# Kernel tuning notes

Hardware: AMD Instinct MI355X
Metric: run time of the kernel (lower is better)

Reference implementation:

```python
import jax, jax.numpy as jnp
import numpy as np

N, M, K = 262144, 65536, 32
C_IN, C_OUT = 64, 128
BN_EPS = 1e-5


def setup_inputs() -> dict:
    key = jax.random.key(0)
    ks = jax.random.split(key, 6)
    p = jax.random.normal(ks[0], (N, 3), jnp.float32)
    x = jax.random.normal(ks[1], (N, C_IN), jnp.float32)
    o = jnp.array([N], jnp.int32)  # single-cloud batch offsets
    idx = jnp.sort(jax.random.randint(ks[2], (M,), 0, N))  # sampled point indices (FPS stand-in)
    knn_idx = jax.random.randint(ks[3], (M, K), 0, N)      # neighbor indices (ball-query/knn stand-in)
    # learned params: Linear(C_IN+3 -> C_OUT) + BatchNorm1d(C_OUT)
    W = jax.random.normal(ks[4], (C_IN + 3, C_OUT), jnp.float32) / np.sqrt(C_IN + 3).astype(np.float32)
    b = jnp.zeros((C_OUT,), jnp.float32)
    gamma = jnp.ones((C_OUT,), jnp.float32)
    beta = jnp.zeros((C_OUT,), jnp.float32)
    return dict(p=p, x=x, o=o, idx=idx, knn_idx=knn_idx, W=W, b=b, gamma=gamma, beta=beta)


def reference(p, x, o, idx, knn_idx, W, b, gamma, beta):
    # sampler: n_p = p[idx]
    n_p = p[idx]  # [M, 3]
    # pooling with with_xyz=True: gather K neighbors, concat relative xyz, max-pool over K
    rel = p[knn_idx] - n_p[:, None, :]                      # [M, K, 3]
    grouped = jnp.concatenate([rel, x[knn_idx]], axis=-1)   # [M, K, 3+C_IN]
    pooled = grouped.max(axis=1)                            # [M, 3+C_IN]
    # convs: Linear -> BatchNorm1d (training-mode batch stats) -> ReLU
    h = pooled @ W + b                                      # [M, C_OUT]
    mean = h.mean(axis=0)
    var = h.var(axis=0)
    h = (h - mean) * jax.lax.rsqrt(var + BN_EPS) * gamma + beta
    x_out = jnp.maximum(h, 0.0)
    n_o = jnp.array([idx.shape[0]], jnp.int32)
    return (n_p, x_out, n_o)
```

## Files before the change

### kernel.cpp

```cpp
#include <hip/hip_runtime.h>
#include <hip/hip_fp16.h>
#include <math.h>

#define K_NB  32
#define C_IN  64
#define C_OUT 128
#define KP    96
#define TILE  128

typedef _Float16 f16x8 __attribute__((ext_vector_type(8)));
typedef float    f32x4 __attribute__((ext_vector_type(4)));

__device__ __forceinline__ float2 u2f2(unsigned u) {
    __half2 h = *reinterpret_cast<__half2*>(&u);
    return __half22float2(h);
}
__device__ __forceinline__ unsigned pk(float a, float b) {
    __half2 h = __floats2half2_rn(a, b);
    return *reinterpret_cast<unsigned*>(&h);
}

__global__ __launch_bounds__(256) void sa_zero(float* __restrict__ g, int n)
{
    for (int i = threadIdx.x; i < n; i += 256) g[i] = 0.f;
}

__global__ __launch_bounds__(256) void sa_cvt(
    const float4* __restrict__ x4, uint2* __restrict__ xh, int n4)
{
    for (int i = blockIdx.x * blockDim.x + threadIdx.x; i < n4;
         i += gridDim.x * blockDim.x) {
        float4 v = x4[i];
        xh[i] = make_uint2(pk(v.x, v.y), pk(v.z, v.w));
    }
}

__global__ __launch_bounds__(256) void sa_pool_h(
    const float* __restrict__ p, const uint4* __restrict__ xh4,
    const int* __restrict__ idx, const int* __restrict__ knn,
    float* __restrict__ np_out, float* __restrict__ hbuf)
{
    const int lane = threadIdx.x & 63;
    const int m    = blockIdx.x * 4 + (threadIdx.x >> 6);

    int kidx = 0;
    if (lane < K_NB) kidx = knn[m * K_NB + lane];

    float mx[8];
    #pragma unroll
    for (int j = 0; j < 8; ++j) mx[j] = -INFINITY;

    const int sub = lane & 7;
    #pragma unroll
    for (int i = 0; i < 4; ++i) {
        int nb = __shfl(kidx, i * 8 + (lane >> 3));
        uint4 u = xh4[(size_t)nb * 8 + sub];
        float2 f0 = u2f2(u.x), f1 = u2f2(u.y), f2 = u2f2(u.z), f3 = u2f2(u.w);
        mx[0] = fmaxf(mx[0], f0.x); mx[1] = fmaxf(mx[1], f0.y);
        mx[2] = fmaxf(mx[2], f1.x); mx[3] = fmaxf(mx[3], f1.y);
        mx[4] = fmaxf(mx[4], f2.x); mx[5] = fmaxf(mx[5], f2.y);
        mx[6] = fmaxf(mx[6], f3.x); mx[7] = fmaxf(mx[7], f3.y);
    }
    #pragma unroll
    for (int off = 8; off <= 32; off <<= 1)
        #pragma unroll
        for (int j = 0; j < 8; ++j)
            mx[j] = fmaxf(mx[j], __shfl_xor(mx[j], off));

    float px = -INFINITY, py = -INFINITY, pz = -INFINITY;
    if (lane < K_NB) {
        const float* pp = p + (size_t)kidx * 3;
        px = pp[0]; py = pp[1]; pz = pp[2];
    }
    #pragma unroll
    for (int off = 32; off >= 1; off >>= 1) {
        px = fmaxf(px, __shfl_xor(px, off));
        py = fmaxf(py, __shfl_xor(py, off));
        pz = fmaxf(pz, __shfl_xor(pz, off));
    }

    const int s = idx[m];
    const float npx = p[(size_t)s*3+0];
    const float npy = p[(size_t)s*3+1];
    const float npz = p[(size_t)s*3+2];
    if (lane < 3) np_out[(size_t)m*3 + lane] = (lane == 0) ? npx : (lane == 1 ? npy : npz);

    const int tile = m >> 7, rl = m & (TILE - 1);
    __half* rowh = (__half*)(hbuf + (size_t)tile * TILE * C_OUT) + rl * KP;
    if (lane < 8) {
        *(uint4*)(rowh + lane * 8) =
            make_uint4(pk(mx[0],mx[1]), pk(mx[2],mx[3]), pk(mx[4],mx[5]), pk(mx[6],mx[7]));
    } else if (lane == 8) {
        *(uint4*)(rowh + 64) = make_uint4(pk(px-npx, py-npy), pk(pz-npz, 0.f), 0u, 0u);
    } else if (lane < 12) {
        *(uint4*)(rowh + 64 + (lane - 8) * 8) = make_uint4(0u, 0u, 0u, 0u);
    }
}

__global__ __launch_bounds__(256) void sa_pool_f(
    const float* __restrict__ p, const float* __restrict__ x,
    const int* __restrict__ idx, const int* __restrict__ knn,
    float* __restrict__ np_out, float* __restrict__ hbuf)
{
    const int lane = threadIdx.x & 63;
    const int m    = blockIdx.x * 4 + (threadIdx.x >> 6);
    int kidx = 0;
    if (lane < K_NB) kidx = knn[m * K_NB + lane];
    float xmax = -INFINITY;
    #pragma unroll
    for (int k = 0; k < K_NB; ++k) {
        int nb = __shfl(kidx, k);
        xmax = fmaxf(xmax, x[(size_t)nb * C_IN + lane]);
    }
    float px = -INFINITY, py = -INFINITY, pz = -INFINITY;
    if (lane < K_NB) {
        const float* pp = p + (size_t)kidx * 3;
        px = pp[0]; py = pp[1]; pz = pp[2];
    }
    #pragma unroll
    for (int off = 32; off >= 1; off >>= 1) {
        px = fmaxf(px, __shfl_xor(px, off));
        py = fmaxf(py, __shfl_xor(py, off));
        pz = fmaxf(pz, __shfl_xor(pz, off));
    }
    const int s = idx[m];
    const float npx = p[(size_t)s*3], npy = p[(size_t)s*3+1], npz = p[(size_t)s*3+2];
    if (lane < 3) np_out[(size_t)m*3 + lane] = (lane == 0) ? npx : (lane == 1 ? npy : npz);

    const int tile = m >> 7, rl = m & (TILE - 1);
    __half* rowh = (__half*)(hbuf + (size_t)tile * TILE * C_OUT) + rl * KP;
    if (lane < 8) {
        float v[8];
        #pragma unroll
        for (int j = 0; j < 8; ++j) v[j] = __shfl(xmax, lane * 8 + j);
        *(uint4*)(rowh + lane * 8) =
            make_uint4(pk(v[0],v[1]), pk(v[2],v[3]), pk(v[4],v[5]), pk(v[6],v[7]));
    } else if (lane == 8) {
        *(uint4*)(rowh + 64) = make_uint4(pk(px-npx, py-npy), pk(pz-npz, 0.f), 0u, 0u);
    } else if (lane < 12) {
        *(uint4*)(rowh + 64 + (lane - 8) * 8) = make_uint4(0u, 0u, 0u, 0u);
    }
}

__global__ __launch_bounds__(256) void sa_gemm_mfma(
    const float* __restrict__ W, const float* __restrict__ bias,
    float* __restrict__ h, float* __restrict__ gsum, unsigned rep_mask)
{
    __shared__ __half Wt[C_OUT][128];
    __shared__ float reds[16][C_OUT];
    __shared__ float redq[16][C_OUT];

    const int t    = threadIdx.x;
    const int wave = t >> 6, lane = t & 63;
    const int l15  = lane & 15, lg = lane >> 4;
    const int m0   = blockIdx.x * TILE;

    for (int e = t; e < C_OUT * KP; e += 256) {
        const int c = e & 127, kk = e >> 7;
        float w = 0.f;
        if (kk < C_IN)          w = W[(size_t)(3 + kk) * C_OUT + c];
        else if (kk < C_IN + 3) w = W[(size_t)(kk - C_IN) * C_OUT + c];
        Wt[c][(((kk >> 3) ^ (c & 7)) << 3) | (kk & 7)] = __float2half(w);
    }

    const __half* tb = (const __half*)(h + (size_t)blockIdx.x * TILE * C_OUT);
    f16x8 A[2][3];
    #pragma unroll
    for (int rt = 0; rt < 2; ++rt) {
        const int rl = wave * 32 + rt * 16 + l15;
        #pragma unroll
        for (int ks = 0; ks < 3; ++ks)
            A[rt][ks] = *(const f16x8*)(tb + (size_t)rl * KP + ks * 32 + lg * 8);
    }
    __syncthreads();

    f32x4 acc[2][8];
    #pragma unroll
    for (int ct = 0; ct < 8; ++ct) {
        const float bc = bias[ct * 16 + l15];
        acc[0][ct] = (f32x4){bc, bc, bc, bc};
        acc[1][ct] = (f32x4){bc, bc, bc, bc};
    }
    #pragma unroll
    for (int ks = 0; ks < 3; ++ks) {
        #pragma unroll
        for (int ct = 0; ct < 8; ++ct) {
            const int c  = ct * 16 + l15;
            const int kc = ks * 4 + lg;
            const f16x8 wf = *(const f16x8*)&Wt[c][((kc ^ (c & 7)) << 3)];
            acc[0][ct] = __builtin_amdgcn_mfma_f32_16x16x32_f16(A[0][ks], wf, acc[0][ct], 0, 0, 0);
            acc[1][ct] = __builtin_amdgcn_mfma_f32_16x16x32_f16(A[1][ks], wf, acc[1][ct], 0, 0, 0);
        }
    }

    float s8[8], q8[8];
    #pragma unroll
    for (int ct = 0; ct < 8; ++ct) { s8[ct] = 0.f; q8[ct] = 0.f; }
    #pragma unroll
    for (int rt = 0; rt < 2; ++rt) {
        #pragma unroll
        for (int ct = 0; ct < 8; ++ct) {
            const int col = ct * 16 + l15;
            #pragma unroll
            for (int r = 0; r < 4; ++r) {
                const int row = m0 + wave * 32 + rt * 16 + lg * 4 + r;
                const float v = acc[rt][ct][r];
                h[(size_t)row * C_OUT + col] = v;
                s8[ct] += v;
                q8[ct]  = fmaf(v, v, q8[ct]);
            }
        }
    }
    #pragma unroll
    for (int ct = 0; ct < 8; ++ct) {
        reds[wave * 4 + lg][ct * 16 + l15] = s8[ct];
        redq[wave * 4 + lg][ct * 16 + l15] = q8[ct];
    }
    __syncthreads();
    if (t < C_OUT) {
        float ss = 0.f, qq = 0.f;
        #pragma unroll
        for (int i = 0; i < 16; ++i) { ss += reds[i][t]; qq += redq[i][t]; }
        float* g = gsum + (size_t)(blockIdx.x & rep_mask) * 2 * C_OUT;
        atomicAdd(&g[t],         ss);
        atomicAdd(&g[C_OUT + t], qq);
    }
}

__global__ __launch_bounds__(128) void sa_finalize(
    const float* __restrict__ gsum, const float* __restrict__ gamma,
    const float* __restrict__ beta, float* __restrict__ ss,
    float* __restrict__ no_out, int M, int rep)
{
    const int j = threadIdx.x;
    float s = 0.f, s2 = 0.f;
    for (int r = 0; r < rep; ++r) {
        s  += gsum[(size_t)r * 2 * C_OUT + j];
        s2 += gsum[(size_t)r * 2 * C_OUT + C_OUT + j];
    }
    const float inv_m = 1.0f / (float)M;
    const float mean = s * inv_m;
    const float var  = fmaf(-mean, mean, s2 * inv_m);
    const float sc   = gamma[j] * rsqrtf(var + 1e-5f);
    ss[j]         = sc;
    ss[C_OUT + j] = fmaf(-mean, sc, beta[j]);
    if (j == 0) no_out[0] = (float)M;
}

__global__ __launch_bounds__(256) void sa_bnrelu(
    float* __restrict__ h, const float* __restrict__ ss, int M)
{
    __shared__ float sc[C_OUT], sh[C_OUT];
    if (threadIdx.x < C_OUT) {
        sc[threadIdx.x] = ss[threadIdx.x];
        sh[threadIdx.x] = ss[C_OUT + threadIdx.x];
    }
    __syncthreads();
    const size_t total4 = (size_t)M * C_OUT / 4;
    float4* h4 = (float4*)h;
    for (size_t i = (size_t)blockIdx.x * blockDim.x + threadIdx.x;
         i < total4; i += (size_t)gridDim.x * blockDim.x) {
        float4 v = h4[i];
        const int c = (int)((i * 4) & (C_OUT - 1));
        v.x = fmaxf(fmaf(v.x, sc[c+0], sh[c+0]), 0.f);
        v.y = fmaxf(fmaf(v.y, sc[c+1], sh[c+1]), 0.f);
        v.z = fmaxf(fmaf(v.z, sc[c+2], sh[c+2]), 0.f);
        v.w = fmaxf(fmaf(v.w, sc[c+3], sh[c+3]), 0.f);
        h4[i] = v;
    }
}

extern "C" void kernel_launch(void* const* d_in, const int* in_sizes, int n_in,
                              void* d_out, int out_size, void* d_ws, size_t ws_size,
                              hipStream_t stream)
{
    const float* p     = (const float*)d_in[0];
    const float* x     = (const float*)d_in[1];
    const int*   idx   = (const int*)d_in[3];
    const int*   knn   = (const int*)d_in[4];
    const float* W     = (const float*)d_in[5];
    const float* bias  = (const float*)d_in[6];
    const float* gamma = (const float*)d_in[7];
    const float* beta  = (const float*)d_in[8];

    const int N = in_sizes[1] / C_IN;
    const int M = in_sizes[3];

    float* out    = (float*)d_out;
    float* np_out = out;
    float* h      = out + (size_t)M * 3;
    float* no_out = out + (size_t)M * 3 + (size_t)M * C_OUT;

    const size_t xh_bytes  = (size_t)N * C_IN * sizeof(__half);
    const bool   fp16_path = ws_size >= xh_bytes + 2048;

    const size_t tail = fp16_path ? (ws_size - xh_bytes) : ws_size;
    int rep = 1;
    while (rep < 64 && (size_t)(2 * rep) * 2 * C_OUT * sizeof(float) + 1024 <= tail)
        rep <<= 1;

    float* gsum = fp16_path ? (float*)((char*)d_ws + xh_bytes) : (float*)d_ws;
    float* ss   = gsum + (size_t)rep * 2 * C_OUT;

    sa_zero<<<1, 256, 0, stream>>>(gsum, rep * 2 * C_OUT);
    if (fp16_path) {
        __half* xh = (__half*)d_ws;
        const int n4 = N * C_IN / 4;
        sa_cvt   <<<2048, 256, 0, stream>>>((const float4*)x, (uint2*)xh, n4);
        sa_pool_h<<<M / 4, 256, 0, stream>>>(p, (const uint4*)xh, idx, knn, np_out, h);
    } else {
        sa_pool_f<<<M / 4, 256, 0, stream>>>(p, x, idx, knn, np_out, h);
    }
    sa_gemm_mfma<<<M / TILE, 256, 0, stream>>>(W, bias, h, gsum, (unsigned)(rep - 1));
    sa_finalize <<<1,        128, 0, stream>>>(gsum, gamma, beta, ss, no_out, M, rep);
    sa_bnrelu   <<<2048,     256, 0, stream>>>(h, ss, M);
}
```

Measured before the change: 130.7 us.

## Fuse zeroing and BN finalize into neighbors, use packed fp16 max in pooling

Folds the gsum zeroing into the fp16 conversion kernel and moves the BN statistics finalize into every block of the BN+ReLU kernel, which removes two tiny launches. The pooling max now runs directly on packed halves with v_pk_max_f16, so there is no fp16-to-fp32 unpack and shuffle traffic is halved. The replica count for the atomic stat buffers is capped at 8 instead of 64, and the BN grid drops to 1024 blocks. The trade-off is that each BN block redundantly re-reduces the stats, and fewer replicas can mean more atomic contention.

```diff
diff --git a/kernel.cpp b/kernel.cpp
--- a/kernel.cpp
+++ b/kernel.cpp
@@ -2,32 +2,38 @@
 #include <hip/hip_fp16.h>
 #include <math.h>
 
-#define K_NB  32
-#define C_IN  64
-#define C_OUT 128
-#define KP    96
-#define TILE  128
+#define K_NB   32
+#define C_IN   64
+#define C_OUT  128
+#define KP     96
+#define TILE   128
+#define BN_EPS 1e-5f
 
 typedef _Float16 f16x8 __attribute__((ext_vector_type(8)));
 typedef float    f32x4 __attribute__((ext_vector_type(4)));
 
-__device__ __forceinline__ float2 u2f2(unsigned u) {
-    __half2 h = *reinterpret_cast<__half2*>(&u);
-    return __half22float2(h);
-}
 __device__ __forceinline__ unsigned pk(float a, float b) {
     __half2 h = __floats2half2_rn(a, b);
     return *reinterpret_cast<unsigned*>(&h);
 }
 
+__device__ __forceinline__ unsigned pkmax(unsigned a, unsigned b) {
+    unsigned d;
+    asm volatile("v_pk_max_f16 %0, %1, %2" : "=v"(d) : "v"(a), "v"(b));
+    return d;
+}
+
 __global__ __launch_bounds__(256) void sa_zero(float* __restrict__ g, int n)
 {
     for (int i = threadIdx.x; i < n; i += 256) g[i] = 0.f;
 }
 
 __global__ __launch_bounds__(256) void sa_cvt(
-    const float4* __restrict__ x4, uint2* __restrict__ xh, int n4)
-{
+    const float4* __restrict__ x4, uint2* __restrict__ xh, int n4,
+    float* __restrict__ gsum, int ng)
+{
+    if (blockIdx.x == 0)
+        for (int i = threadIdx.x; i < ng; i += 256) gsum[i] = 0.f;
     for (int i = blockIdx.x * blockDim.x + threadIdx.x; i < n4;
          i += gridDim.x * blockDim.x) {
         float4 v = x4[i];
@@ -46,26 +52,26 @@
     int kidx = 0;
     if (lane < K_NB) kidx = knn[m * K_NB + lane];
 
-    float mx[8];
-    #pragma unroll
-    for (int j = 0; j < 8; ++j) mx[j] = -INFINITY;
+    unsigned mx0 = 0xFC00FC00u, mx1 = 0xFC00FC00u;
+    unsigned mx2 = 0xFC00FC00u, mx3 = 0xFC00FC00u;
 
     const int sub = lane & 7;
     #pragma unroll
     for (int i = 0; i < 4; ++i) {
         int nb = __shfl(kidx, i * 8 + (lane >> 3));
         uint4 u = xh4[(size_t)nb * 8 + sub];
-        float2 f0 = u2f2(u.x), f1 = u2f2(u.y), f2 = u2f2(u.z), f3 = u2f2(u.w);
-        mx[0] = fmaxf(mx[0], f0.x); mx[1] = fmaxf(mx[1], f0.y);
-        mx[2] = fmaxf(mx[2], f1.x); mx[3] = fmaxf(mx[3], f1.y);
-        mx[4] = fmaxf(mx[4], f2.x); mx[5] = fmaxf(mx[5], f2.y);
-        mx[6] = fmaxf(mx[6], f3.x); mx[7] = fmaxf(mx[7], f3.y);
-    }
-    #pragma unroll
-    for (int off = 8; off <= 32; off <<= 1)
-        #pragma unroll
-        for (int j = 0; j < 8; ++j)
-            mx[j] = fmaxf(mx[j], __shfl_xor(mx[j], off));
+        mx0 = pkmax(mx0, u.x);
+        mx1 = pkmax(mx1, u.y);
+        mx2 = pkmax(mx2, u.z);
+        mx3 = pkmax(mx3, u.w);
+    }
+    #pragma unroll
+    for (int off = 8; off <= 32; off <<= 1) {
+        mx0 = pkmax(mx0, (unsigned)__shfl_xor((int)mx0, off));
+        mx1 = pkmax(mx1, (unsigned)__shfl_xor((int)mx1, off));
+        mx2 = pkmax(mx2, (unsigned)__shfl_xor((int)mx2, off));
+        mx3 = pkmax(mx3, (unsigned)__shfl_xor((int)mx3, off));
+    }
 
     float px = -INFINITY, py = -INFINITY, pz = -INFINITY;
     if (lane < K_NB) {
@@ -88,8 +94,7 @@
     const int tile = m >> 7, rl = m & (TILE - 1);
     __half* rowh = (__half*)(hbuf + (size_t)tile * TILE * C_OUT) + rl * KP;
     if (lane < 8) {
-        *(uint4*)(rowh + lane * 8) =
-            make_uint4(pk(mx[0],mx[1]), pk(mx[2],mx[3]), pk(mx[4],mx[5]), pk(mx[6],mx[7]));
+        *(uint4*)(rowh + lane * 8) = make_uint4(mx0, mx1, mx2, mx3);
     } else if (lane == 8) {
         *(uint4*)(rowh + 64) = make_uint4(pk(px-npx, py-npy), pk(pz-npz, 0.f), 0u, 0u);
     } else if (lane < 12) {
@@ -227,38 +232,32 @@
     }
 }
 
-__global__ __launch_bounds__(128) void sa_finalize(
-    const float* __restrict__ gsum, const float* __restrict__ gamma,
-    const float* __restrict__ beta, float* __restrict__ ss,
+__global__ __launch_bounds__(256) void sa_bnrelu_fin(
+    float* __restrict__ h, const float* __restrict__ gsum,
+    const float* __restrict__ gamma, const float* __restrict__ beta,
     float* __restrict__ no_out, int M, int rep)
 {
-    const int j = threadIdx.x;
-    float s = 0.f, s2 = 0.f;
-    for (int r = 0; r < rep; ++r) {
-        s  += gsum[(size_t)r * 2 * C_OUT + j];
-        s2 += gsum[(size_t)r * 2 * C_OUT + C_OUT + j];
-    }
-    const float inv_m = 1.0f / (float)M;
-    const float mean = s * inv_m;
-    const float var  = fmaf(-mean, mean, s2 * inv_m);
-    const float sc   = gamma[j] * rsqrtf(var + 1e-5f);
-    ss[j]         = sc;
-    ss[C_OUT + j] = fmaf(-mean, sc, beta[j]);
-    if (j == 0) no_out[0] = (float)M;
-}
-
-__global__ __launch_bounds__(256) void sa_bnrelu(
-    float* __restrict__ h, const float* __restrict__ ss, int M)
-{
     __shared__ float sc[C_OUT], sh[C_OUT];
-    if (threadIdx.x < C_OUT) {
-        sc[threadIdx.x] = ss[threadIdx.x];
-        sh[threadIdx.x] = ss[C_OUT + threadIdx.x];
-    }
+    const int t = threadIdx.x;
+    if (t < C_OUT) {
+        float s = 0.f, s2 = 0.f;
+        for (int r = 0; r < rep; ++r) {
+            s  += gsum[(size_t)r * 2 * C_OUT + t];
+            s2 += gsum[(size_t)r * 2 * C_OUT + C_OUT + t];
+        }
+        const float inv_m = 1.0f / (float)M;
+        const float mean = s * inv_m;
+        const float var  = fmaf(-mean, mean, s2 * inv_m);
+        const float scv  = gamma[t] * rsqrtf(var + BN_EPS);
+        sc[t] = scv;
+        sh[t] = fmaf(-mean, scv, beta[t]);
+    }
+    if (blockIdx.x == 0 && t == 0) no_out[0] = (float)M;
     __syncthreads();
+
     const size_t total4 = (size_t)M * C_OUT / 4;
     float4* h4 = (float4*)h;
-    for (size_t i = (size_t)blockIdx.x * blockDim.x + threadIdx.x;
+    for (size_t i = (size_t)blockIdx.x * blockDim.x + t;
          i < total4; i += (size_t)gridDim.x * blockDim.x) {
         float4 v = h4[i];
         const int c = (int)((i * 4) & (C_OUT - 1));
@@ -296,22 +295,23 @@
 
     const size_t tail = fp16_path ? (ws_size - xh_bytes) : ws_size;
     int rep = 1;
-    while (rep < 64 && (size_t)(2 * rep) * 2 * C_OUT * sizeof(float) + 1024 <= tail)
+    while (rep < 8 && (size_t)(2 * rep) * 2 * C_OUT * sizeof(float) <= tail)
         rep <<= 1;
 
     float* gsum = fp16_path ? (float*)((char*)d_ws + xh_bytes) : (float*)d_ws;
-    float* ss   = gsum + (size_t)rep * 2 * C_OUT;
-
-    sa_zero<<<1, 256, 0, stream>>>(gsum, rep * 2 * C_OUT);
+    const unsigned rep_mask = (unsigned)(rep - 1);
+
     if (fp16_path) {
         __half* xh = (__half*)d_ws;
         const int n4 = N * C_IN / 4;
-        sa_cvt   <<<2048, 256, 0, stream>>>((const float4*)x, (uint2*)xh, n4);
+        sa_cvt   <<<2048, 256, 0, stream>>>((const float4*)x, (uint2*)xh, n4,
+                                            gsum, rep * 2 * C_OUT);
         sa_pool_h<<<M / 4, 256, 0, stream>>>(p, (const uint4*)xh, idx, knn, np_out, h);
     } else {
+        sa_zero  <<<1, 256, 0, stream>>>(gsum, rep * 2 * C_OUT);
         sa_pool_f<<<M / 4, 256, 0, stream>>>(p, x, idx, knn, np_out, h);
     }
-    sa_gemm_mfma<<<M / TILE, 256, 0, stream>>>(W, bias, h, gsum, (unsigned)(rep - 1));
-    sa_finalize <<<1,        128, 0, stream>>>(gsum, gamma, beta, ss, no_out, M, rep);
-    sa_bnrelu   <<<2048,     256, 0, stream>>>(h, ss, M);
-}
+
+    sa_gemm_mfma <<<M / TILE, 256, 0, stream>>>(W, bias, h, gsum, rep_mask);
+    sa_bnrelu_fin<<<1024,     256, 0, stream>>>(h, gsum, gamma, beta, no_out, M, rep);
+}
```

Measured after the change: 112.2 us. -14.2%, faster.
